# Optimization experiments

Hardware: AMD Instinct MI355X
Metric: run time of the kernel (lower is better)

## Reference

```python
import jax, jax.numpy as jnp
import numpy as np

N, E, D_IN, HID, D_OUT = 200000, 5000000, 128, 16, 2


def setup_inputs() -> dict:
    key = jax.random.key(0)
    ks = jax.random.split(key, 8)
    x = jax.random.normal(ks[0], (N, D_IN), dtype=jnp.float32)
    edge_index = jax.random.randint(ks[1], (2, E), 0, N, dtype=jnp.int32)
    W1 = jax.random.normal(ks[2], (D_IN, HID), dtype=jnp.float32) / np.sqrt(D_IN)
    b1 = jnp.zeros((HID,), dtype=jnp.float32)
    W3 = jax.random.normal(ks[3], (HID, HID), dtype=jnp.float32) / np.sqrt(HID)
    b3 = jnp.zeros((HID,), dtype=jnp.float32)
    W2 = jax.random.normal(ks[4], (HID, D_OUT), dtype=jnp.float32) / np.sqrt(HID)
    b2 = jnp.zeros((D_OUT,), dtype=jnp.float32)
    return {"x": x, "edge_index": edge_index, "W1": W1, "b1": b1,
            "W3": W3, "b3": b3, "W2": W2, "b2": b2}


def reference(x, edge_index, W1, b1, W3, b3, W2, b2):
    # GCNConv: add self-loops, symmetric normalization, aggregate, linear+bias.
    src, dst = edge_index[0], edge_index[1]
    loops = jnp.arange(N, dtype=src.dtype)
    src_f = jnp.concatenate([src, loops])  # [E+N]
    dst_f = jnp.concatenate([dst, loops])
    deg = jax.ops.segment_sum(jnp.ones_like(src_f, dtype=jnp.float32), dst_f,
                              num_segments=N)
    dis = jnp.where(deg > 0, jax.lax.rsqrt(jnp.maximum(deg, 1.0)), 0.0)
    norm = dis[src_f] * dis[dst_f]  # [E+N]

    def gcn_conv(h, W, b):
        h = h @ W                                   # [N, F_out] small GEMM
        msg = h[src_f] * norm[:, None]              # gather + scale
        agg = jax.ops.segment_sum(msg, dst_f, num_segments=N)  # scatter-add
        return agg + b

    h = jax.nn.relu(gcn_conv(x, W1, b1))    # conv1 (dropout is identity in eval)
    h = jax.nn.relu(gcn_conv(h, W3, b3))    # conv3 loop (conv_number-2 = 1 iter)
    h = gcn_conv(h, W2, b2)                 # conv2
    return jax.nn.log_softmax(h, axis=1)
```

## Files before the change

kernel.cpp:

```cpp
#include <hip/hip_runtime.h>

#define NN 200000
#define NE 5000000
#define DIN 128
#define HID 16
#define DOUT 2
#define BSZ 391
#define NB 512
#define LBITS 9
#define NCH 8
#define SLICE_DIV 25000
#define NK (NB * NCH)
#define PB 256
#define PT 512
#define CAP 2048

static_assert((size_t)NB * BSZ >= NN, "bucket coverage");
static_assert((NN - 1) / SLICE_DIV == NCH - 1, "slice count");


__global__ __launch_bounds__(PT) void hist_pass(const int* __restrict__ src,
                                                const int* __restrict__ dst,
                                                int* __restrict__ blockHist) {
    __shared__ int h[NK];
    for (int k = threadIdx.x; k < NK; k += PT) h[k] = 0;
    __syncthreads();
    for (int i = blockIdx.x * PT + threadIdx.x; i < NE; i += PB * PT) {
        int dv = dst[i];
        int sv = src[i];
        atomicAdd(&h[((dv / BSZ) << 3) + sv / SLICE_DIV], 1);
    }
    __syncthreads();
    for (int k = threadIdx.x; k < NK; k += PT)
        blockHist[(size_t)blockIdx.x * NK + k] = h[k];
}

__global__ __launch_bounds__(256) void tot_pass(const int* __restrict__ blockHist,
                                                int* __restrict__ chunkStart) {
    int k = blockIdx.x * 256 + threadIdx.x;
    if (k >= NK) return;
    int s = 0;
#pragma unroll 8
    for (int b = 0; b < PB; ++b) s += blockHist[(size_t)b * NK + k];
    chunkStart[k] = s;
}

__global__ __launch_bounds__(1024) void scan_keys(int* __restrict__ chunkStart) {
    __shared__ int psum[1024];
    int t = threadIdx.x;
    const int KPT = (NK + 1023) / 1024;
    int k0 = t * KPT; if (k0 > NK) k0 = NK;
    int k1 = k0 + KPT; if (k1 > NK) k1 = NK;
    int vals[KPT];
    int s = 0;
    for (int k = k0; k < k1; ++k) { vals[k - k0] = chunkStart[k]; s += vals[k - k0]; }
    psum[t] = s;
    __syncthreads();
    for (int off = 1; off < 1024; off <<= 1) {
        int add = (t >= off) ? psum[t - off] : 0;
        __syncthreads();
        psum[t] += add;
        __syncthreads();
    }
    int run = psum[t] - s;
    for (int k = k0; k < k1; ++k) { chunkStart[k] = run; run += vals[k - k0]; }
    if (t == 0) chunkStart[NK] = NE;
}

__global__ __launch_bounds__(256) void offsets_pass(int* __restrict__ blockHist,
                                                    const int* __restrict__ chunkStart) {
    int k = blockIdx.x * 256 + threadIdx.x;
    if (k >= NK) return;
    int r = chunkStart[k];
#pragma unroll 8
    for (int b = 0; b < PB; ++b) {
        size_t idx = (size_t)b * NK + k;
        int v = blockHist[idx];
        blockHist[idx] = r;
        r += v;
    }
}

__global__ __launch_bounds__(PT) void scatter_pass(const int* __restrict__ src,
                                                   const int* __restrict__ dst,
                                                   const int* __restrict__ blockHist,
                                                   unsigned* __restrict__ pedge) {
    __shared__ int cur[NK];
    for (int k = threadIdx.x; k < NK; k += PT)
        cur[k] = blockHist[(size_t)blockIdx.x * NK + k];
    __syncthreads();
    for (int i = blockIdx.x * PT + threadIdx.x; i < NE; i += PB * PT) {
        int sv = src[i];
        int dv = dst[i];
        int bk = dv / BSZ;
        int key = (bk << 3) + sv / SLICE_DIV;
        int pos = atomicAdd(&cur[key], 1);
        pedge[pos] = ((unsigned)sv << LBITS) | (unsigned)(dv - bk * BSZ);
    }
}


__global__ __launch_bounds__(512) void subsort(const unsigned* __restrict__ pedge,
                                               const int* __restrict__ chunkStart,
                                               int* __restrict__ pedge2,
                                               int* __restrict__ rowStart,
                                               float* __restrict__ dis) {
    __shared__ unsigned ebuf[CAP];
    __shared__ int hist[512];
    __shared__ int cur[512];
    __shared__ int wsum[8];
    int t = threadIdx.x;
    int b = blockIdx.x;
    int lane = t & 63, w = t >> 6;
    int deg = 1;
    const unsigned LM = (1u << LBITS) - 1u;
    for (int s = 0; s < NCH; ++s) {
        int seg = b * NCH + s;
        int e0 = chunkStart[seg], e1 = chunkStart[seg + 1];
        int n = e1 - e0;
        hist[t] = 0;
        __syncthreads();
        for (int i = t; i < n; i += 512) {
            unsigned p = pedge[e0 + i];
            ebuf[i] = p;
            atomicAdd(&hist[p & LM], 1);
        }
        __syncthreads();
        int v = hist[t];
        deg += v;
        int inc = v;
        for (int off = 1; off < 64; off <<= 1) {
            int nb = __shfl_up(inc, off, 64);
            if (lane >= off) inc += nb;
        }
        if (lane == 63) wsum[w] = inc;
        __syncthreads();
        if (t == 0) {
            int car = 0;
#pragma unroll
            for (int i = 0; i < 8; ++i) { int u = wsum[i]; wsum[i] = car; car += u; }
        }
        __syncthreads();
        int excl = inc - v + wsum[w];
        if (t < BSZ) rowStart[(size_t)seg * BSZ + t] = e0 + excl;
        cur[t] = excl;
        __syncthreads();
        for (int i = t; i < n; i += 512) {
            unsigned p = ebuf[i];
            int pos = atomicAdd(&cur[p & LM], 1);
            pedge2[e0 + pos] = (int)(p >> LBITS);
        }
        __syncthreads();
    }
    int node = b * BSZ + t;
    if (t < BSZ && node < NN) dis[node] = rsqrtf((float)deg);
    if (b == 0 && t == 0) rowStart[(size_t)NK * BSZ] = NE;
}


#define GXR 64
#define XPAD 132
__global__ __launch_bounds__(256) void gemm_x_w1(const float* __restrict__ x,
                                                 const float* __restrict__ W,
                                                 const float* __restrict__ dis,
                                                 float* __restrict__ out) {
    __shared__ float w[DIN * HID];
    __shared__ float xt[GXR * XPAD];
    int t = threadIdx.x;
    for (int i = t; i < DIN * HID; i += 256) w[i] = W[i];
    int rbase = blockIdx.x * GXR;
    const float4* xg = reinterpret_cast<const float4*>(x + (size_t)rbase * DIN);
    float4* xt4 = reinterpret_cast<float4*>(xt);
    for (int i = t; i < GXR * (DIN / 4); i += 256) {
        int row = i >> 5, kk = i & 31;
        xt4[row * (XPAD / 4) + kk] = xg[i];
    }
    __syncthreads();
    int row = t >> 2;
    int c0 = (t & 3) * 4;
    const float* xr = xt + row * XPAD;
    float ax = 0.f, ay = 0.f, az = 0.f, aw = 0.f;
#pragma unroll 4
    for (int k = 0; k < DIN; ++k) {
        float xv = xr[k];
        float4 wv = *reinterpret_cast<const float4*>(&w[k * HID + c0]);
        ax += xv * wv.x; ay += xv * wv.y; az += xv * wv.z; aw += xv * wv.w;
    }
    int node = rbase + row;
    float dd = dis[node];
    *reinterpret_cast<float4*>(&out[(size_t)node * HID + c0]) =
        make_float4(ax * dd, ay * dd, az * dd, aw * dd);
}

__global__ __launch_bounds__(256) void gemm_h_w16(const float* __restrict__ h,
                                                  const float* __restrict__ W,
                                                  const float* __restrict__ dis,
                                                  float* __restrict__ out) {
    __shared__ float w[HID * HID];
    if (threadIdx.x < HID * HID) w[threadIdx.x] = W[threadIdx.x];
    __syncthreads();
    int row = blockIdx.x * 16 + (threadIdx.x >> 4);
    int c = threadIdx.x & 15;
    if (row >= NN) return;
    const float4* hr = reinterpret_cast<const float4*>(h + (size_t)row * HID);
    float acc = 0.f;
#pragma unroll
    for (int k4 = 0; k4 < HID / 4; ++k4) {
        float4 v = hr[k4];
        acc += v.x * w[(4 * k4 + 0) * HID + c] + v.y * w[(4 * k4 + 1) * HID + c]
             + v.z * w[(4 * k4 + 2) * HID + c] + v.w * w[(4 * k4 + 3) * HID + c];
    }
    out[row * HID + c] = acc * dis[row];
}

__global__ __launch_bounds__(256) void gemm_h_w2(const float* __restrict__ h,
                                                 const float* __restrict__ W,
                                                 const float* __restrict__ dis,
                                                 float* __restrict__ out) {
    int t = blockIdx.x * 256 + threadIdx.x;
    int row = t >> 1;
    int c = t & 1;
    if (row >= NN) return;
    const float* hr = h + (size_t)row * HID;
    float acc = 0.f;
#pragma unroll
    for (int k = 0; k < HID; ++k) acc += hr[k] * W[k * DOUT + c];
    out[row * DOUT + c] = acc * dis[row];
}


__device__ __forceinline__ void acc_edges(const int* __restrict__ pedge2,
                                          const float4* __restrict__ xs4,
                                          int e0, int e1, int c4, float4& a) {
    int e = e0;
    for (; e + 1 < e1; e += 2) {
        int s0 = pedge2[e];
        int s1 = pedge2[e + 1];
        float4 u = xs4[(s0 << 2) + c4];
        float4 w = xs4[(s1 << 2) + c4];
        a.x += u.x + w.x; a.y += u.y + w.y; a.z += u.z + w.z; a.w += u.w + w.w;
    }
    if (e < e1) {
        float4 u = xs4[(pedge2[e] << 2) + c4];
        a.x += u.x; a.y += u.y; a.z += u.z; a.w += u.w;
    }
}

__device__ __forceinline__ void store_row(float4* buf4, const float* dis, int node,
                                          int c4, const float4& a, const float4& bb,
                                          int relu) {
    float dd = dis[node];
    float4 v = make_float4(dd * a.x + bb.x, dd * a.y + bb.y,
                           dd * a.z + bb.z, dd * a.w + bb.w);
    if (relu) { v.x = fmaxf(v.x, 0.f); v.y = fmaxf(v.y, 0.f);
                v.z = fmaxf(v.z, 0.f); v.w = fmaxf(v.w, 0.f); }
    buf4[(node << 2) + c4] = v;
}

__global__ __launch_bounds__(1024, 8) void agg16_all(const int* __restrict__ pedge2,
                                                     const int* __restrict__ rowStart,
                                                     const float* __restrict__ xs,
                                                     const float* __restrict__ dis,
                                                     const float* __restrict__ bias,
                                                     float* __restrict__ buf,
                                                     int relu) {
    int t = threadIdx.x;
    int b = blockIdx.x;
    int base = b * BSZ;
    int c4 = t & 3;
    int g = t >> 2;
    const float4* xs4 = reinterpret_cast<const float4*>(xs);
    float4* buf4 = reinterpret_cast<float4*>(buf);
    int d1 = g + 256;
    int n0 = base + g, n1 = base + d1;
    bool r0 = (g < BSZ) && (n0 < NN);
    bool r1 = (d1 < BSZ) && (n1 < NN);
    float4 a0 = make_float4(0.f, 0.f, 0.f, 0.f);
    float4 a1 = a0;
    if (r0) a0 = xs4[(n0 << 2) + c4];
    if (r1) a1 = xs4[(n1 << 2) + c4];
    for (int r = 0; r < NCH; ++r) {
        const int* rs = rowStart + (size_t)(b * NCH + r) * BSZ;
        if (r0) acc_edges(pedge2, xs4, rs[g], rs[g + 1], c4, a0);
        if (r1) acc_edges(pedge2, xs4, rs[d1], rs[d1 + 1], c4, a1);
    }
    float4 bb = reinterpret_cast<const float4*>(bias)[c4];
    if (r0) store_row(buf4, dis, n0, c4, a0, bb, relu);
    if (r1) store_row(buf4, dis, n1, c4, a1, bb, relu);
}

__global__ __launch_bounds__(512) void agg2_lsm(const int* __restrict__ pedge2,
                                                const int* __restrict__ rowStart,
                                                const float* __restrict__ xs,
                                                const float* __restrict__ dis,
                                                const float* __restrict__ bias,
                                                float* __restrict__ out) {
    int t = threadIdx.x;
    int b = blockIdx.x;
    if (t >= BSZ) return;
    int node = b * BSZ + t;
    if (node >= NN) return;
    const float2* xs2 = reinterpret_cast<const float2*>(xs);
    float a0 = 0.f, a1 = 0.f;
    for (int s = 0; s < NCH; ++s) {
        const int* rs = rowStart + (size_t)(b * NCH + s) * BSZ;
        int e0 = rs[t], e1 = rs[t + 1];
        for (int e = e0; e < e1; ++e) {
            float2 v = xs2[pedge2[e]];
            a0 += v.x; a1 += v.y;
        }
    }
    float2 sv = xs2[node];
    float d = dis[node];
    float v0 = (a0 + sv.x) * d + bias[0];
    float v1 = (a1 + sv.y) * d + bias[1];
    float m = fmaxf(v0, v1);
    float lse = m + logf(__expf(v0 - m) + __expf(v1 - m));
    reinterpret_cast<float2*>(out)[node] = make_float2(v0 - lse, v1 - lse);
}


extern "C" void kernel_launch(void* const* d_in, const int* in_sizes, int n_in,
                              void* d_out, int out_size, void* d_ws, size_t ws_size,
                              hipStream_t stream) {
    const float* x = (const float*)d_in[0];
    const int* ei = (const int*)d_in[1];
    const float* W1 = (const float*)d_in[2];
    const float* b1 = (const float*)d_in[3];
    const float* W3 = (const float*)d_in[4];
    const float* b3 = (const float*)d_in[5];
    const float* W2 = (const float*)d_in[6];
    const float* b2 = (const float*)d_in[7];
    float* out = (float*)d_out;

    const int* src = ei;
    const int* dst = ei + NE;

    int* W = (int*)d_ws;
    unsigned* pedge = (unsigned*)W;
    int* pedge2 = W + NE;
    int* rowStart = W + 2 * (size_t)NE;
    int* blockHist = rowStart + (size_t)NK * BSZ + 4;
    int* chunkStart = blockHist + (size_t)PB * NK;
    float* dis = (float*)(chunkStart + NK + 4);
    float* bufB = dis + NN;
    float* bufA = (float*)W;

    const int B = 256;
    auto cdiv = [](long long a, long long b) { return (int)((a + b - 1) / b); };

    hist_pass<<<PB, PT, 0, stream>>>(src, dst, blockHist);
    tot_pass<<<cdiv(NK, 256), 256, 0, stream>>>(blockHist, chunkStart);
    scan_keys<<<1, 1024, 0, stream>>>(chunkStart);
    offsets_pass<<<cdiv(NK, 256), 256, 0, stream>>>(blockHist, chunkStart);
    scatter_pass<<<PB, PT, 0, stream>>>(src, dst, blockHist, pedge);
    subsort<<<NB, 512, 0, stream>>>(pedge, chunkStart, pedge2, rowStart, dis);

    gemm_x_w1<<<NN / GXR, B, 0, stream>>>(x, W1, dis, bufA);
    agg16_all<<<NB, 1024, 0, stream>>>(pedge2, rowStart, bufA, dis, b1, bufB, 1);

    gemm_h_w16<<<cdiv(NN, 16), B, 0, stream>>>(bufB, W3, dis, bufA);
    agg16_all<<<NB, 1024, 0, stream>>>(pedge2, rowStart, bufA, dis, b3, bufB, 1);

    gemm_h_w2<<<cdiv((long long)NN * DOUT, B), B, 0, stream>>>(bufB, W2, dis, bufA);
    agg2_lsm<<<NB, 512, 0, stream>>>(pedge2, rowStart, bufA, dis, b2, out);
}
```

Baseline: 326.7 us.

## Double rows per thread in x@W1 GEMM and unroll edge gathers by four

The first GEMM now processes 128 rows per block, with each thread computing two rows so every W load from shared memory is reused, and a tail guard is added. The 16-wide aggregation replaces the fixed two-nodes-per-group assignment with a contiguous node range per 4-lane group, and its edge loop is unrolled by four to keep more independent gathers in flight. The 2-wide aggregation gets the same four-way unroll. The trade-offs are higher register pressure, more shared memory in the GEMM, and possible load imbalance from serial per-node loops.

```diff
diff --git a/kernel.cpp b/kernel.cpp
--- a/kernel.cpp
+++ b/kernel.cpp
@@ -158,7 +158,7 @@
 }
 
 
-#define GXR 64
+#define GXR 128
 #define XPAD 132
 __global__ __launch_bounds__(256) void gemm_x_w1(const float* __restrict__ x,
                                                  const float* __restrict__ W,
@@ -169,27 +169,39 @@
     int t = threadIdx.x;
     for (int i = t; i < DIN * HID; i += 256) w[i] = W[i];
     int rbase = blockIdx.x * GXR;
+    int nrows = NN - rbase; if (nrows > GXR) nrows = GXR;
     const float4* xg = reinterpret_cast<const float4*>(x + (size_t)rbase * DIN);
     float4* xt4 = reinterpret_cast<float4*>(xt);
-    for (int i = t; i < GXR * (DIN / 4); i += 256) {
+    for (int i = t; i < nrows * (DIN / 4); i += 256) {
         int row = i >> 5, kk = i & 31;
         xt4[row * (XPAD / 4) + kk] = xg[i];
     }
     __syncthreads();
-    int row = t >> 2;
+    int row0 = t >> 2;
+    int row1 = row0 + 64;
     int c0 = (t & 3) * 4;
-    const float* xr = xt + row * XPAD;
-    float ax = 0.f, ay = 0.f, az = 0.f, aw = 0.f;
+    const float* xr0 = xt + row0 * XPAD;
+    const float* xr1 = xt + row1 * XPAD;
+    float4 A0 = make_float4(0.f, 0.f, 0.f, 0.f);
+    float4 A1 = A0;
 #pragma unroll 4
     for (int k = 0; k < DIN; ++k) {
-        float xv = xr[k];
         float4 wv = *reinterpret_cast<const float4*>(&w[k * HID + c0]);
-        ax += xv * wv.x; ay += xv * wv.y; az += xv * wv.z; aw += xv * wv.w;
-    }
-    int node = rbase + row;
-    float dd = dis[node];
-    *reinterpret_cast<float4*>(&out[(size_t)node * HID + c0]) =
-        make_float4(ax * dd, ay * dd, az * dd, aw * dd);
+        float x0 = xr0[k], x1 = xr1[k];
+        A0.x += x0 * wv.x; A0.y += x0 * wv.y; A0.z += x0 * wv.z; A0.w += x0 * wv.w;
+        A1.x += x1 * wv.x; A1.y += x1 * wv.y; A1.z += x1 * wv.z; A1.w += x1 * wv.w;
+    }
+    int n0 = rbase + row0, n1 = rbase + row1;
+    if (n0 < NN) {
+        float dd = dis[n0];
+        *reinterpret_cast<float4*>(&out[(size_t)n0 * HID + c0]) =
+            make_float4(A0.x * dd, A0.y * dd, A0.z * dd, A0.w * dd);
+    }
+    if (n1 < NN) {
+        float dd = dis[n1];
+        *reinterpret_cast<float4*>(&out[(size_t)n1 * HID + c0]) =
+            make_float4(A1.x * dd, A1.y * dd, A1.z * dd, A1.w * dd);
+    }
 }
 
 __global__ __launch_bounds__(256) void gemm_h_w16(const float* __restrict__ h,
@@ -231,30 +243,23 @@
 
 __device__ __forceinline__ void acc_edges(const int* __restrict__ pedge2,
                                           const float4* __restrict__ xs4,
-                                          int e0, int e1, int c4, float4& a) {
-    int e = e0;
-    for (; e + 1 < e1; e += 2) {
-        int s0 = pedge2[e];
-        int s1 = pedge2[e + 1];
-        float4 u = xs4[(s0 << 2) + c4];
-        float4 w = xs4[(s1 << 2) + c4];
-        a.x += u.x + w.x; a.y += u.y + w.y; a.z += u.z + w.z; a.w += u.w + w.w;
-    }
-    if (e < e1) {
+                                          int e, int e1, int c4, float4& a) {
+    for (; e + 3 < e1; e += 4) {
+        int s0 = pedge2[e], s1 = pedge2[e + 1];
+        int s2 = pedge2[e + 2], s3 = pedge2[e + 3];
+        float4 u0 = xs4[(s0 << 2) + c4];
+        float4 u1 = xs4[(s1 << 2) + c4];
+        float4 u2 = xs4[(s2 << 2) + c4];
+        float4 u3 = xs4[(s3 << 2) + c4];
+        a.x += (u0.x + u1.x) + (u2.x + u3.x);
+        a.y += (u0.y + u1.y) + (u2.y + u3.y);
+        a.z += (u0.z + u1.z) + (u2.z + u3.z);
+        a.w += (u0.w + u1.w) + (u2.w + u3.w);
+    }
+    for (; e < e1; ++e) {
         float4 u = xs4[(pedge2[e] << 2) + c4];
         a.x += u.x; a.y += u.y; a.z += u.z; a.w += u.w;
     }
-}
-
-__device__ __forceinline__ void store_row(float4* buf4, const float* dis, int node,
-                                          int c4, const float4& a, const float4& bb,
-                                          int relu) {
-    float dd = dis[node];
-    float4 v = make_float4(dd * a.x + bb.x, dd * a.y + bb.y,
-                           dd * a.z + bb.z, dd * a.w + bb.w);
-    if (relu) { v.x = fmaxf(v.x, 0.f); v.y = fmaxf(v.y, 0.f);
-                v.z = fmaxf(v.z, 0.f); v.w = fmaxf(v.w, 0.f); }
-    buf4[(node << 2) + c4] = v;
 }
 
 __global__ __launch_bounds__(1024, 8) void agg16_all(const int* __restrict__ pedge2,
@@ -268,25 +273,27 @@
     int b = blockIdx.x;
     int base = b * BSZ;
     int c4 = t & 3;
-    int g = t >> 2;
+    int q = t >> 2;
+    int g0 = (q * BSZ) >> 8;
+    int g1 = ((q + 1) * BSZ) >> 8;
     const float4* xs4 = reinterpret_cast<const float4*>(xs);
     float4* buf4 = reinterpret_cast<float4*>(buf);
-    int d1 = g + 256;
-    int n0 = base + g, n1 = base + d1;
-    bool r0 = (g < BSZ) && (n0 < NN);
-    bool r1 = (d1 < BSZ) && (n1 < NN);
-    float4 a0 = make_float4(0.f, 0.f, 0.f, 0.f);
-    float4 a1 = a0;
-    if (r0) a0 = xs4[(n0 << 2) + c4];
-    if (r1) a1 = xs4[(n1 << 2) + c4];
-    for (int r = 0; r < NCH; ++r) {
-        const int* rs = rowStart + (size_t)(b * NCH + r) * BSZ;
-        if (r0) acc_edges(pedge2, xs4, rs[g], rs[g + 1], c4, a0);
-        if (r1) acc_edges(pedge2, xs4, rs[d1], rs[d1 + 1], c4, a1);
-    }
     float4 bb = reinterpret_cast<const float4*>(bias)[c4];
-    if (r0) store_row(buf4, dis, n0, c4, a0, bb, relu);
-    if (r1) store_row(buf4, dis, n1, c4, a1, bb, relu);
+    for (int g = g0; g < g1; ++g) {
+        int node = base + g;
+        if (node >= NN) break;
+        float4 a = xs4[(node << 2) + c4];
+        for (int r = 0; r < NCH; ++r) {
+            const int* rs = rowStart + (size_t)(b * NCH + r) * BSZ;
+            acc_edges(pedge2, xs4, rs[g], rs[g + 1], c4, a);
+        }
+        float dd = dis[node];
+        float4 v = make_float4(dd * a.x + bb.x, dd * a.y + bb.y,
+                               dd * a.z + bb.z, dd * a.w + bb.w);
+        if (relu) { v.x = fmaxf(v.x, 0.f); v.y = fmaxf(v.y, 0.f);
+                    v.z = fmaxf(v.z, 0.f); v.w = fmaxf(v.w, 0.f); }
+        buf4[(node << 2) + c4] = v;
+    }
 }
 
 __global__ __launch_bounds__(512) void agg2_lsm(const int* __restrict__ pedge2,
@@ -304,8 +311,15 @@
     float a0 = 0.f, a1 = 0.f;
     for (int s = 0; s < NCH; ++s) {
         const int* rs = rowStart + (size_t)(b * NCH + s) * BSZ;
-        int e0 = rs[t], e1 = rs[t + 1];
-        for (int e = e0; e < e1; ++e) {
+        int e = rs[t], e1 = rs[t + 1];
+        for (; e + 3 < e1; e += 4) {
+            int s0 = pedge2[e], s1 = pedge2[e + 1];
+            int s2 = pedge2[e + 2], s3 = pedge2[e + 3];
+            float2 v0 = xs2[s0], v1 = xs2[s1], v2 = xs2[s2], v3 = xs2[s3];
+            a0 += (v0.x + v1.x) + (v2.x + v3.x);
+            a1 += (v0.y + v1.y) + (v2.y + v3.y);
+        }
+        for (; e < e1; ++e) {
             float2 v = xs2[pedge2[e]];
             a0 += v.x; a1 += v.y;
         }
@@ -356,7 +370,7 @@
     scatter_pass<<<PB, PT, 0, stream>>>(src, dst, blockHist, pedge);
     subsort<<<NB, 512, 0, stream>>>(pedge, chunkStart, pedge2, rowStart, dis);
 
-    gemm_x_w1<<<NN / GXR, B, 0, stream>>>(x, W1, dis, bufA);
+    gemm_x_w1<<<cdiv(NN, GXR), B, 0, stream>>>(x, W1, dis, bufA);
     agg16_all<<<NB, 1024, 0, stream>>>(pedge2, rowStart, bufA, dis, b1, bufB, 1);
 
     gemm_h_w16<<<cdiv(NN, 16), B, 0, stream>>>(bufB, W3, dis, bufA);
```

Result: slower. 338.7 us (+3.7%).
